# Optimization experiments

Measured on AMD Instinct MI355X. Metric: run time of the kernel, lower is better.

Reference implementation:

```python
import jax, jax.numpy as jnp
import numpy as np

NUM_HEADS = 12
SPARSITY = 0.5

def setup_inputs() -> dict:
    key = jax.random.key(0)
    ks = jax.random.split(key, 5)
    B, N, C = 16, 577, 768
    x = jax.random.normal(ks[0], (B, N, C), dtype=jnp.float32)
    x_original = jax.random.normal(ks[1], (B, N, C), dtype=jnp.float32)
    qkv_w = jax.random.normal(ks[2], (3 * C, C), dtype=jnp.float32) * (C ** -0.5)
    proj_w = jax.random.normal(ks[3], (C, C), dtype=jnp.float32) * (C ** -0.5)
    proj_b = jax.random.normal(ks[4], (C,), dtype=jnp.float32) * 0.01
    return {"x": x, "x_original": x_original, "qkv_w": qkv_w,
            "proj_w": proj_w, "proj_b": proj_b, "num_prop": 57}

def reference(x, x_original, qkv_w, proj_w, proj_b, num_prop):
    B, N, C = x.shape
    H = NUM_HEADS
    hd = C // H
    scale = hd ** -0.5
    # qkv projection (no bias): [B,N,3C] -> q,k,v each [B,H,N,hd]
    qkv = (x @ qkv_w.T).reshape(B, N, 3, H, hd).transpose(2, 0, 3, 1, 4)
    q, k, v = qkv[0], qkv[1], qkv[2]
    attn = jax.nn.softmax(jnp.einsum('bhnd,bhmd->bhnm', q * scale, k), axis=-1)
    # sparsity threshold: keep entries >= the int(N*N*sparsity)-th largest per (b,h)
    if SPARSITY < 1:
        flat = attn.reshape(B, H, N * N)
        desc = -jnp.sort(-flat, axis=-1)  # descending
        sigma = desc[:, :, int(N * N * SPARSITY)][:, :, None, None]
        attn = jnp.where(attn >= sigma, attn, jnp.zeros((), attn.dtype))
    if num_prop > 0:
        K = N - num_prop  # tokens kept (incl. CLS)
        # token importance: max over heads of attention diagonal (excluding CLS)
        diag = jnp.diagonal(attn, axis1=-2, axis2=-1)[:, :, 1:]  # [B,H,N-1]
        token_rank = jnp.argsort(-diag.max(axis=1), axis=1)      # [B,N-1] desc
        index_kept = token_rank[:, :N - 1 - num_prop] + 1        # [B,K-1]
        index_kept = jnp.concatenate(
            [jnp.zeros((B, 1), index_kept.dtype), index_kept], axis=1)  # [B,K]
        # gather kept query rows of attn: [B,H,K,N]
        idx = jnp.broadcast_to(index_kept[:, None, :, None], (B, H, K, N))
        attn_kept = jnp.take_along_axis(attn, idx, axis=2)
        x_original = jnp.take_along_axis(
            x_original, jnp.broadcast_to(index_kept[:, :, None], (B, K, C)), axis=1)
        out = jnp.einsum('bhkn,bhnd->bhkd', attn_kept, v)
        out = out.transpose(0, 2, 1, 3).reshape(B, K, C)
    else:
        out = jnp.einsum('bhnm,bhmd->bhnd', attn, v)
        out = out.transpose(0, 2, 1, 3).reshape(B, N, C)
    out = out @ proj_w.T + proj_b
    return (out, x_original)
```

## Files before the change

### kernel.cpp

```cpp
#include <hip/hip_runtime.h>
#include <cstdint>
#include <cstddef>


namespace {
constexpr int B_  = 16;
constexpr int N_  = 577;
constexpr int C_  = 768;
constexpr int H_  = 12;
constexpr int HD_ = 64;
constexpr int BH_ = B_ * H_;
constexpr int KK_ = N_ - 57;
constexpr unsigned KIDX_ = 166464u;
constexpr int M1_ = B_ * N_;
constexpr int M2_ = B_ * KK_;
}

__global__ __launch_bounds__(256) void qkv_gemm(
    const float* __restrict__ X, const float* __restrict__ W,
    float* __restrict__ qb, float* __restrict__ kb, float* __restrict__ vb) {
  __shared__ float Xs[64][37];
  __shared__ float Ws2[128][37];
  const int m0 = blockIdx.x * 64;
  const int n0 = blockIdx.y * 128;
  const int t = threadIdx.x;
  const int tx = t & 15, ty = t >> 4;
  const int sc = t & 7, sr = t >> 3;
  float acc[4][8] = {};
  for (int k0 = 0; k0 < 768; k0 += 32) {
    __syncthreads();
#pragma unroll
    for (int s = 0; s < 2; s++) {
      int r = sr + 32 * s;
      int gm = m0 + r;
      float4 v = make_float4(0.f, 0.f, 0.f, 0.f);
      if (gm < M1_) v = *(const float4*)&X[(size_t)gm * 768 + k0 + 4 * sc];
      Xs[r][4*sc+0] = v.x; Xs[r][4*sc+1] = v.y;
      Xs[r][4*sc+2] = v.z; Xs[r][4*sc+3] = v.w;
    }
#pragma unroll
    for (int s = 0; s < 4; s++) {
      int r = sr + 32 * s;
      float4 v = *(const float4*)&W[(size_t)(n0 + r) * 768 + k0 + 4 * sc];
      Ws2[r][4*sc+0] = v.x; Ws2[r][4*sc+1] = v.y;
      Ws2[r][4*sc+2] = v.z; Ws2[r][4*sc+3] = v.w;
    }
    __syncthreads();
#pragma unroll 8
    for (int kk = 0; kk < 32; kk++) {
      float a[4], bb[8];
#pragma unroll
      for (int i = 0; i < 4; i++) a[i] = Xs[tx + 16*i][kk];
#pragma unroll
      for (int j = 0; j < 8; j++) bb[j] = Ws2[8*ty + j][kk];
#pragma unroll
      for (int i = 0; i < 4; i++)
#pragma unroll
        for (int j = 0; j < 8; j++) acc[i][j] = __builtin_fmaf(a[i], bb[j], acc[i][j]);
    }
  }
  for (int i = 0; i < 4; i++) {
    int gm = m0 + tx + 16*i;
    if (gm >= M1_) continue;
    int b = gm / N_, n = gm % N_;
    for (int j = 0; j < 8; j++) {
      int gn = n0 + 8*ty + j;
      int which = gn / C_, rem = gn % C_;
      int h = rem >> 6, d = rem & 63;
      float* dst = (which == 0) ? qb : (which == 1) ? kb : vb;
      dst[(((size_t)(b * H_ + h)) * N_ + n) * HD_ + d] = acc[i][j];
    }
  }
}

__global__ __launch_bounds__(256) void attn_stats(
    const float* __restrict__ qb, const float* __restrict__ kb,
    float* __restrict__ rowmax_g, float* __restrict__ rowsum_g,
    float* __restrict__ ldiag) {
  __shared__ float Qs[64][69];
  __shared__ float Ksf[128 * 69];
  const int bh = blockIdx.x;
  const int q0 = blockIdx.y * 64;
  const int t = threadIdx.x;
  const int tx = t & 15, ty = t >> 4;
  {
    const int c = t & 15, r0 = t >> 4;
#pragma unroll
    for (int s = 0; s < 4; s++) {
      int r = r0 + 16 * s;
      int gq = q0 + r;
      float4 v = make_float4(0.f, 0.f, 0.f, 0.f);
      if (gq < N_) v = *(const float4*)&qb[((size_t)bh * N_ + gq) * HD_ + 4 * c];
      Qs[r][4*c+0] = v.x * 0.125f; Qs[r][4*c+1] = v.y * 0.125f;
      Qs[r][4*c+2] = v.z * 0.125f; Qs[r][4*c+3] = v.w * 0.125f;
    }
  }
  float m[4], ss[4];
#pragma unroll
  for (int i = 0; i < 4; i++) { m[i] = -INFINITY; ss[i] = 0.f; }
  for (int n0 = 0; n0 < N_; n0 += 128) {
    __syncthreads();
    {
      const int c = t & 15, r0 = t >> 4;
#pragma unroll
      for (int s = 0; s < 8; s++) {
        int r = r0 + 16 * s;
        int gn = n0 + r;
        float4 v = make_float4(0.f, 0.f, 0.f, 0.f);
        if (gn < N_) v = *(const float4*)&kb[((size_t)bh * N_ + gn) * HD_ + 4 * c];
        float* kr = &Ksf[r * 69];
        kr[4*c+0] = v.x; kr[4*c+1] = v.y; kr[4*c+2] = v.z; kr[4*c+3] = v.w;
      }
    }
    __syncthreads();
    float l[4][8];
#pragma unroll
    for (int i = 0; i < 4; i++)
#pragma unroll
      for (int j = 0; j < 8; j++) l[i][j] = 0.f;
#pragma unroll 8
    for (int d = 0; d < 64; d++) {
      float a[4], bb[8];
#pragma unroll
      for (int i = 0; i < 4; i++) a[i] = Qs[tx + 16*i][d];
#pragma unroll
      for (int j = 0; j < 8; j++) bb[j] = Ksf[(8*ty + j) * 69 + d];
#pragma unroll
      for (int i = 0; i < 4; i++)
#pragma unroll
        for (int j = 0; j < 8; j++) l[i][j] = __builtin_fmaf(a[i], bb[j], l[i][j]);
    }
    int cbase = n0 + 8 * ty;
    int cv = N_ - cbase; if (cv > 8) cv = 8;
    if (cv > 0) {
#pragma unroll
      for (int i = 0; i < 4; i++) {
        int gq = q0 + tx + 16*i;
        if (gq >= N_) continue;
        float tmax = -INFINITY;
        for (int j = 0; j < 8; j++) if (j < cv) tmax = fmaxf(tmax, l[i][j]);
        float mn = fmaxf(m[i], tmax);
        ss[i] *= expf(m[i] - mn);
        for (int j = 0; j < 8; j++) if (j < cv) ss[i] += expf(l[i][j] - mn);
        m[i] = mn;
        int dj = gq - cbase;
        if (dj >= 0 && dj < cv) ldiag[(size_t)bh * N_ + gq] = l[i][dj];
      }
    }
  }
  __syncthreads();
  float* Mred = Ksf;
  float* Sred = Ksf + 1024;
#pragma unroll
  for (int i = 0; i < 4; i++) {
    int row = tx + 16*i;
    Mred[row * 16 + ty] = m[i];
    Sred[row * 16 + ty] = ss[i];
  }
  __syncthreads();
  if (t < 64) {
    int gq = q0 + t;
    if (gq < N_) {
      float M = -INFINITY;
      for (int k = 0; k < 16; k++) M = fmaxf(M, Mred[t*16 + k]);
      float S = 0.f;
      for (int k = 0; k < 16; k++) S += expf(Mred[t*16+k] - M) * Sred[t*16+k];
      rowmax_g[(size_t)bh * N_ + gq] = M;
      rowsum_g[(size_t)bh * N_ + gq] = S;
    }
  }
}

template <int MODE>
__global__ __launch_bounds__(256) void hist_pass(
    const float* __restrict__ qb, const float* __restrict__ kb,
    const float* __restrict__ rowmax_g, const float* __restrict__ rowsum_g,
    const unsigned* __restrict__ pfx_in, unsigned* __restrict__ hist_out) {
  constexpr int HB = (MODE == 2) ? 256 : 4096;
  __shared__ float Qs[64][69];
  __shared__ float Ksf[128 * 69];
  __shared__ unsigned hloc[HB];
  const int bh = blockIdx.x;
  const int q0 = blockIdx.y * 64;
  const int t = threadIdx.x;
  const int tx = t & 15, ty = t >> 4;
  for (int i = t; i < HB; i += 256) hloc[i] = 0u;
  const unsigned pf = (MODE == 0) ? 0u : pfx_in[bh];
  {
    const int c = t & 15, r0 = t >> 4;
#pragma unroll
    for (int s = 0; s < 4; s++) {
      int r = r0 + 16 * s;
      int gq = q0 + r;
      float4 v = make_float4(0.f, 0.f, 0.f, 0.f);
      if (gq < N_) v = *(const float4*)&qb[((size_t)bh * N_ + gq) * HD_ + 4 * c];
      Qs[r][4*c+0] = v.x * 0.125f; Qs[r][4*c+1] = v.y * 0.125f;
      Qs[r][4*c+2] = v.z * 0.125f; Qs[r][4*c+3] = v.w * 0.125f;
    }
  }
  float M[4], inv[4];
#pragma unroll
  for (int i = 0; i < 4; i++) {
    int gq = q0 + tx + 16*i;
    if (gq < N_) {
      M[i] = rowmax_g[(size_t)bh * N_ + gq];
      inv[i] = 1.f / rowsum_g[(size_t)bh * N_ + gq];
    } else { M[i] = 0.f; inv[i] = 0.f; }
  }
  for (int n0 = 0; n0 < N_; n0 += 128) {
    __syncthreads();
    {
      const int c = t & 15, r0 = t >> 4;
#pragma unroll
      for (int s = 0; s < 8; s++) {
        int r = r0 + 16 * s;
        int gn = n0 + r;
        float4 v = make_float4(0.f, 0.f, 0.f, 0.f);
        if (gn < N_) v = *(const float4*)&kb[((size_t)bh * N_ + gn) * HD_ + 4 * c];
        float* kr = &Ksf[r * 69];
        kr[4*c+0] = v.x; kr[4*c+1] = v.y; kr[4*c+2] = v.z; kr[4*c+3] = v.w;
      }
    }
    __syncthreads();
    float l[4][8];
#pragma unroll
    for (int i = 0; i < 4; i++)
#pragma unroll
      for (int j = 0; j < 8; j++) l[i][j] = 0.f;
#pragma unroll 8
    for (int d = 0; d < 64; d++) {
      float a[4], bb[8];
#pragma unroll
      for (int i = 0; i < 4; i++) a[i] = Qs[tx + 16*i][d];
#pragma unroll
      for (int j = 0; j < 8; j++) bb[j] = Ksf[(8*ty + j) * 69 + d];
#pragma unroll
      for (int i = 0; i < 4; i++)
#pragma unroll
        for (int j = 0; j < 8; j++) l[i][j] = __builtin_fmaf(a[i], bb[j], l[i][j]);
    }
    int cbase = n0 + 8 * ty;
#pragma unroll
    for (int i = 0; i < 4; i++) {
      int gq = q0 + tx + 16 * i;
#pragma unroll
      for (int j = 0; j < 8; j++) {
        bool valid = (gq < N_) && (cbase + j < N_);
        if (MODE == 0) {
          unsigned bin = 0xFFFFu;
          if (valid) {
            float e = expf(l[i][j] - M[i]);
            float v = e * inv[i];
            bin = __float_as_uint(v) >> 20;
          }
          unsigned lead = (unsigned)__builtin_amdgcn_readfirstlane((int)bin);
          unsigned long long mm = __ballot(bin == lead);
          if (bin == lead) {
            if (lead != 0xFFFFu && (t & 63) == (__ffsll((unsigned long long)mm) - 1))
              atomicAdd(&hloc[lead], (unsigned)__popcll(mm));
          } else if (bin != 0xFFFFu) {
            atomicAdd(&hloc[bin], 1u);
          }
        } else if (valid) {
          float e = expf(l[i][j] - M[i]);
          float v = e * inv[i];
          unsigned bits = __float_as_uint(v);
          if (MODE == 1) {
            if ((bits >> 20) == pf) atomicAdd(&hloc[(bits >> 8) & 0xFFFu], 1u);
          } else {
            if ((bits >> 8) == pf) atomicAdd(&hloc[bits & 0xFFu], 1u);
          }
        }
      }
    }
  }
  __syncthreads();
  for (int i = t; i < HB; i += 256)
    if (hloc[i]) atomicAdd(&hist_out[(size_t)bh * HB + i], hloc[i]);
}

__global__ __launch_bounds__(64) void select_level(
    const unsigned* __restrict__ hist, int nbins,
    const unsigned* __restrict__ krem_in, const unsigned* __restrict__ pfx_in,
    unsigned* __restrict__ krem_out, unsigned* __restrict__ pfx_out, int shift) {
  const int bh = blockIdx.x;
  const int l = threadIdx.x;
  const int seg = nbins / 64;
  const unsigned krem = krem_in ? krem_in[bh] : KIDX_;
  const unsigned* hb = hist + (size_t)bh * nbins;
  __shared__ unsigned ps[64];
  unsigned psum = 0;
  int hi = nbins - 1 - l * seg;
  for (int i = 0; i < seg; i++) psum += hb[hi - i];
  ps[l] = psum;
  __syncthreads();
  if (l == 0) {
    unsigned cum = 0, before = 0;
    int bin = 0;
    for (int j = 0; j < 64; j++) {
      if (cum + ps[j] > krem) {
        unsigned c = cum;
        int hj = nbins - 1 - j * seg;
        for (int i = 0; i < seg; i++) {
          unsigned cnt = hb[hj - i];
          if (c + cnt > krem) { bin = hj - i; before = c; break; }
          c += cnt;
        }
        break;
      }
      cum += ps[j];
    }
    unsigned p = pfx_in ? pfx_in[bh] : 0u;
    pfx_out[bh] = (p << shift) | (unsigned)bin;
    krem_out[bh] = krem - before;
  }
}

__global__ __launch_bounds__(576) void rank_kernel(
    const float* __restrict__ ldiag, const float* __restrict__ rowmax_g,
    const float* __restrict__ rowsum_g, const unsigned* __restrict__ sigbits,
    int* __restrict__ kept) {
  const int b = blockIdx.x;
  const int i = threadIdx.x;
  __shared__ float sc[576];
  float s = 0.f;
  for (int h = 0; h < H_; h++) {
    int bh = b * H_ + h;
    float l = ldiag[(size_t)bh * N_ + (i + 1)];
    float M = rowmax_g[(size_t)bh * N_ + (i + 1)];
    float inv = 1.f / rowsum_g[(size_t)bh * N_ + (i + 1)];
    float e = expf(l - M);
    float v = e * inv;
    float sg = __uint_as_float(sigbits[bh]);
    if (v >= sg) s = fmaxf(s, v);
  }
  sc[i] = s;
  __syncthreads();
  int r = 0;
  for (int j = 0; j < 576; j++) {
    float sj = sc[j];
    if (sj > s || (sj == s && j < i)) r++;
  }
  if (r < KK_ - 1) kept[b * KK_ + r + 1] = i + 1;
  if (i == 0) kept[b * KK_] = 0;
}

__global__ __launch_bounds__(256) void gather_x(
    const float* __restrict__ xo, const int* __restrict__ kept,
    float* __restrict__ out2) {
  const int bp = blockIdx.x;
  const int b = bp / KK_, p = bp % KK_;
  const int src = kept[b * KK_ + p];
  const float* s = xo + ((size_t)b * N_ + src) * C_;
  float* d = out2 + (size_t)bp * C_;
  for (int c = threadIdx.x; c < C_; c += 256) d[c] = s[c];
}

__global__ __launch_bounds__(256) void av_kernel(
    const float* __restrict__ qb, const float* __restrict__ kb,
    const float* __restrict__ vb, const int* __restrict__ kept,
    const float* __restrict__ rowmax_g, const float* __restrict__ rowsum_g,
    const unsigned* __restrict__ sigbits, float* __restrict__ out1) {
  __shared__ float Qs[64][69];
  __shared__ float Ksf[64 * 69];
  __shared__ float Vs[64][69];
  __shared__ int ridx[64];
  __shared__ float Ml[64], Il[64];
  const int bh = blockIdx.x;
  const int p0 = blockIdx.y * 64;
  const int b = bh / H_, h = bh % H_;
  const float sigma = __uint_as_float(sigbits[bh]);
  const int t = threadIdx.x;
  const int tx = t & 15, ty = t >> 4;
  if (t < 64) {
    int pp = p0 + t;
    int r = (pp < KK_) ? kept[b * KK_ + pp] : 0;
    ridx[t] = r;
    Ml[t] = rowmax_g[(size_t)bh * N_ + r];
    Il[t] = 1.f / rowsum_g[(size_t)bh * N_ + r];
  }
  __syncthreads();
  {
    const int c = t & 15, r0 = t >> 4;
#pragma unroll
    for (int s = 0; s < 4; s++) {
      int r = r0 + 16 * s;
      int gq = ridx[r];
      float4 v = *(const float4*)&qb[((size_t)bh * N_ + gq) * HD_ + 4 * c];
      Qs[r][4*c+0] = v.x * 0.125f; Qs[r][4*c+1] = v.y * 0.125f;
      Qs[r][4*c+2] = v.z * 0.125f; Qs[r][4*c+3] = v.w * 0.125f;
    }
  }
  float M[4], inv[4];
#pragma unroll
  for (int i = 0; i < 4; i++) { int row = tx + 16*i; M[i] = Ml[row]; inv[i] = Il[row]; }
  float acc[4][4] = {};
  for (int n0 = 0; n0 < N_; n0 += 64) {
    __syncthreads();
    {
      const int c = t & 15, r0 = t >> 4;
#pragma unroll
      for (int s = 0; s < 4; s++) {
        int r = r0 + 16 * s;
        int gn = n0 + r;
        float4 kv = make_float4(0.f, 0.f, 0.f, 0.f);
        float4 vv = make_float4(0.f, 0.f, 0.f, 0.f);
        if (gn < N_) {
          kv = *(const float4*)&kb[((size_t)bh * N_ + gn) * HD_ + 4 * c];
          vv = *(const float4*)&vb[((size_t)bh * N_ + gn) * HD_ + 4 * c];
        }
        float* kr = &Ksf[r * 69];
        kr[4*c+0] = kv.x; kr[4*c+1] = kv.y; kr[4*c+2] = kv.z; kr[4*c+3] = kv.w;
        Vs[r][4*c+0] = vv.x; Vs[r][4*c+1] = vv.y;
        Vs[r][4*c+2] = vv.z; Vs[r][4*c+3] = vv.w;
      }
    }
    __syncthreads();
    float l[4][4];
#pragma unroll
    for (int i = 0; i < 4; i++)
#pragma unroll
      for (int j = 0; j < 4; j++) l[i][j] = 0.f;
#pragma unroll 8
    for (int d = 0; d < 64; d++) {
      float a[4], bb[4];
#pragma unroll
      for (int i = 0; i < 4; i++) a[i] = Qs[tx + 16*i][d];
#pragma unroll
      for (int j = 0; j < 4; j++) bb[j] = Ksf[(4*ty + j) * 69 + d];
#pragma unroll
      for (int i = 0; i < 4; i++)
#pragma unroll
        for (int j = 0; j < 4; j++) l[i][j] = __builtin_fmaf(a[i], bb[j], l[i][j]);
    }
    __syncthreads();
#pragma unroll
    for (int i = 0; i < 4; i++) {
#pragma unroll
      for (int j = 0; j < 4; j++) {
        float e = expf(l[i][j] - M[i]);
        float v = e * inv[i];
        float pm = (v >= sigma) ? v : 0.f;
        Ksf[(tx + 16*i) * 69 + 4*ty + j] = pm;
      }
    }
    __syncthreads();
#pragma unroll 8
    for (int n = 0; n < 64; n++) {
      float pa[4], vv[4];
#pragma unroll
      for (int i = 0; i < 4; i++) pa[i] = Ksf[(tx + 16*i) * 69 + n];
#pragma unroll
      for (int j = 0; j < 4; j++) vv[j] = Vs[n][4*ty + j];
#pragma unroll
      for (int i = 0; i < 4; i++)
#pragma unroll
        for (int j = 0; j < 4; j++) acc[i][j] = __builtin_fmaf(pa[i], vv[j], acc[i][j]);
    }
  }
#pragma unroll
  for (int i = 0; i < 4; i++) {
    int pp = p0 + tx + 16*i;
    if (pp >= KK_) continue;
#pragma unroll
    for (int j = 0; j < 4; j++) {
      out1[((size_t)(b * KK_ + pp)) * C_ + h * HD_ + 4*ty + j] = acc[i][j];
    }
  }
}

__global__ __launch_bounds__(256) void proj_gemm(
    const float* __restrict__ Xi, const float* __restrict__ W,
    const float* __restrict__ bias, float* __restrict__ out) {
  __shared__ float Xs[64][37];
  __shared__ float Ws2[128][37];
  const int m0 = blockIdx.x * 64;
  const int n0 = blockIdx.y * 128;
  const int t = threadIdx.x;
  const int tx = t & 15, ty = t >> 4;
  const int sc = t & 7, sr = t >> 3;
  float acc[4][8] = {};
  for (int k0 = 0; k0 < 768; k0 += 32) {
    __syncthreads();
#pragma unroll
    for (int s = 0; s < 2; s++) {
      int r = sr + 32 * s;
      float4 v = *(const float4*)&Xi[(size_t)(m0 + r) * 768 + k0 + 4 * sc];
      Xs[r][4*sc+0] = v.x; Xs[r][4*sc+1] = v.y;
      Xs[r][4*sc+2] = v.z; Xs[r][4*sc+3] = v.w;
    }
#pragma unroll
    for (int s = 0; s < 4; s++) {
      int r = sr + 32 * s;
      float4 v = *(const float4*)&W[(size_t)(n0 + r) * 768 + k0 + 4 * sc];
      Ws2[r][4*sc+0] = v.x; Ws2[r][4*sc+1] = v.y;
      Ws2[r][4*sc+2] = v.z; Ws2[r][4*sc+3] = v.w;
    }
    __syncthreads();
#pragma unroll 8
    for (int kk = 0; kk < 32; kk++) {
      float a[4], bb[8];
#pragma unroll
      for (int i = 0; i < 4; i++) a[i] = Xs[tx + 16*i][kk];
#pragma unroll
      for (int j = 0; j < 8; j++) bb[j] = Ws2[8*ty + j][kk];
#pragma unroll
      for (int i = 0; i < 4; i++)
#pragma unroll
        for (int j = 0; j < 8; j++) acc[i][j] = __builtin_fmaf(a[i], bb[j], acc[i][j]);
    }
  }
  for (int i = 0; i < 4; i++) {
    int gm = m0 + tx + 16*i;
    for (int j = 0; j < 8; j++) {
      int gn = n0 + 8*ty + j;
      out[(size_t)gm * C_ + gn] = acc[i][j] + bias[gn];
    }
  }
}

extern "C" void kernel_launch(void* const* d_in, const int* in_sizes, int n_in,
                              void* d_out, int out_size, void* d_ws, size_t ws_size,
                              hipStream_t stream) {
  (void)in_sizes; (void)n_in; (void)out_size; (void)ws_size;
  const float* x    = (const float*)d_in[0];
  const float* xo   = (const float*)d_in[1];
  const float* qkvw = (const float*)d_in[2];
  const float* pw   = (const float*)d_in[3];
  const float* pb   = (const float*)d_in[4];

  char* ws = (char*)d_ws;
  size_t off = 0;
  auto alloc = [&](size_t bytes) -> char* {
    char* p = ws + off;
    off += (bytes + 255) & ~(size_t)255;
    return p;
  };
  const size_t szQ    = (size_t)BH_ * N_ * HD_ * 4;
  const size_t szOut1 = (size_t)M2_ * C_ * 4;
  const size_t szRow  = (size_t)BH_ * N_ * 4;
  const size_t szH12  = (size_t)BH_ * 4096 * 4;
  const size_t szH3   = (size_t)BH_ * 256 * 4;

  float* qb     = (float*)alloc(szQ);
  float* kb     = (float*)alloc(szQ);
  float* vb     = (float*)alloc(szQ);
  float* out1   = (float*)alloc(szOut1);
  float* ldiag  = (float*)alloc(szRow);
  float* rowmax = (float*)alloc(szRow);
  float* rowsum = (float*)alloc(szRow);
  unsigned* hist1 = (unsigned*)alloc(szH12);
  unsigned* hist2 = (unsigned*)alloc(szH12);
  unsigned* hist3 = (unsigned*)alloc(szH3);
  unsigned* pfx1  = (unsigned*)alloc(BH_ * 4);
  unsigned* krem1 = (unsigned*)alloc(BH_ * 4);
  unsigned* pfx2  = (unsigned*)alloc(BH_ * 4);
  unsigned* krem2 = (unsigned*)alloc(BH_ * 4);
  unsigned* pfx3  = (unsigned*)alloc(BH_ * 4);
  unsigned* krem3 = (unsigned*)alloc(BH_ * 4);
  int* kept       = (int*)alloc((size_t)B_ * KK_ * 4);

  hipMemsetAsync(hist1, 0, szH12, stream);
  hipMemsetAsync(hist2, 0, szH12, stream);
  hipMemsetAsync(hist3, 0, szH3, stream);

  qkv_gemm<<<dim3(145, 18), 256, 0, stream>>>(x, qkvw, qb, kb, vb);
  attn_stats<<<dim3(BH_, 10), 256, 0, stream>>>(qb, kb, rowmax, rowsum, ldiag);
  hist_pass<0><<<dim3(BH_, 10), 256, 0, stream>>>(qb, kb, rowmax, rowsum, nullptr, hist1);
  select_level<<<BH_, 64, 0, stream>>>(hist1, 4096, nullptr, nullptr, krem1, pfx1, 12);
  hist_pass<1><<<dim3(BH_, 10), 256, 0, stream>>>(qb, kb, rowmax, rowsum, pfx1, hist2);
  select_level<<<BH_, 64, 0, stream>>>(hist2, 4096, krem1, pfx1, krem2, pfx2, 12);
  hist_pass<2><<<dim3(BH_, 10), 256, 0, stream>>>(qb, kb, rowmax, rowsum, pfx2, hist3);
  select_level<<<BH_, 64, 0, stream>>>(hist3, 256, krem2, pfx2, krem3, pfx3, 8);
  rank_kernel<<<B_, 576, 0, stream>>>(ldiag, rowmax, rowsum, pfx3, kept);

  float* outp = (float*)d_out;
  gather_x<<<M2_, 256, 0, stream>>>(xo, kept, outp + (size_t)M2_ * C_);
  av_kernel<<<dim3(BH_, 9), 256, 0, stream>>>(qb, kb, vb, kept, rowmax, rowsum, pfx3, out1);
  proj_gemm<<<dim3(130, 6), 256, 0, stream>>>(out1, pw, pb, outp);
}
```

Before: 1.983 ms.

## Vectorize shared-memory tiles with float4 loads across all GEMM-like kernels

Changes shared-memory tiles from odd-padded (37/69) rows to 16-byte aligned rows of 68 floats, so global-to-shared stores and inner-loop reads use float4. The thread-to-column mapping becomes strided (ty + 16*j) instead of contiguous, and the QKV/proj GEMMs now step K by 64 instead of 32. The aim is fewer LDS instructions per FMA in the QK^T, PV and projection loops. Float4 reads with a 68-float stride can cause LDS bank conflicts, and the changed reduction order may shift numerics slightly.

```diff
diff --git a/kernel.cpp b/kernel.cpp
--- a/kernel.cpp
+++ b/kernel.cpp
@@ -16,55 +16,62 @@
 constexpr int M2_ = B_ * KK_;
 }
 
+__device__ __forceinline__ void fma4(const float4& a, const float4& b, float& acc) {
+  acc = __builtin_fmaf(a.x, b.x, acc);
+  acc = __builtin_fmaf(a.y, b.y, acc);
+  acc = __builtin_fmaf(a.z, b.z, acc);
+  acc = __builtin_fmaf(a.w, b.w, acc);
+}
+
 __global__ __launch_bounds__(256) void qkv_gemm(
     const float* __restrict__ X, const float* __restrict__ W,
     float* __restrict__ qb, float* __restrict__ kb, float* __restrict__ vb) {
-  __shared__ float Xs[64][37];
-  __shared__ float Ws2[128][37];
+  __shared__ __align__(16) float Xs[64][68];
+  __shared__ __align__(16) float Ws2[128][68];
   const int m0 = blockIdx.x * 64;
   const int n0 = blockIdx.y * 128;
   const int t = threadIdx.x;
   const int tx = t & 15, ty = t >> 4;
-  const int sc = t & 7, sr = t >> 3;
   float acc[4][8] = {};
-  for (int k0 = 0; k0 < 768; k0 += 32) {
-    __syncthreads();
-#pragma unroll
-    for (int s = 0; s < 2; s++) {
-      int r = sr + 32 * s;
-      int gm = m0 + r;
-      float4 v = make_float4(0.f, 0.f, 0.f, 0.f);
-      if (gm < M1_) v = *(const float4*)&X[(size_t)gm * 768 + k0 + 4 * sc];
-      Xs[r][4*sc+0] = v.x; Xs[r][4*sc+1] = v.y;
-      Xs[r][4*sc+2] = v.z; Xs[r][4*sc+3] = v.w;
-    }
-#pragma unroll
-    for (int s = 0; s < 4; s++) {
-      int r = sr + 32 * s;
-      float4 v = *(const float4*)&W[(size_t)(n0 + r) * 768 + k0 + 4 * sc];
-      Ws2[r][4*sc+0] = v.x; Ws2[r][4*sc+1] = v.y;
-      Ws2[r][4*sc+2] = v.z; Ws2[r][4*sc+3] = v.w;
-    }
-    __syncthreads();
-#pragma unroll 8
-    for (int kk = 0; kk < 32; kk++) {
-      float a[4], bb[8];
-#pragma unroll
-      for (int i = 0; i < 4; i++) a[i] = Xs[tx + 16*i][kk];
-#pragma unroll
-      for (int j = 0; j < 8; j++) bb[j] = Ws2[8*ty + j][kk];
+  for (int k0 = 0; k0 < 768; k0 += 64) {
+    __syncthreads();
+    {
+      const int c = t & 15, r0 = t >> 4;
+#pragma unroll
+      for (int s = 0; s < 4; s++) {
+        int r = r0 + 16 * s;
+        int gm = m0 + r;
+        float4 v = make_float4(0.f, 0.f, 0.f, 0.f);
+        if (gm < M1_) v = *(const float4*)&X[(size_t)gm * 768 + k0 + 4 * c];
+        *(float4*)&Xs[r][4 * c] = v;
+      }
+#pragma unroll
+      for (int s = 0; s < 8; s++) {
+        int r = r0 + 16 * s;
+        float4 v = *(const float4*)&W[(size_t)(n0 + r) * 768 + k0 + 4 * c];
+        *(float4*)&Ws2[r][4 * c] = v;
+      }
+    }
+    __syncthreads();
+#pragma unroll 2
+    for (int d4 = 0; d4 < 16; d4++) {
+      float4 a4[4], b4[8];
+#pragma unroll
+      for (int i = 0; i < 4; i++) a4[i] = *(const float4*)&Xs[tx + 16 * i][4 * d4];
+#pragma unroll
+      for (int j = 0; j < 8; j++) b4[j] = *(const float4*)&Ws2[ty + 16 * j][4 * d4];
 #pragma unroll
       for (int i = 0; i < 4; i++)
 #pragma unroll
-        for (int j = 0; j < 8; j++) acc[i][j] = __builtin_fmaf(a[i], bb[j], acc[i][j]);
+        for (int j = 0; j < 8; j++) fma4(a4[i], b4[j], acc[i][j]);
     }
   }
   for (int i = 0; i < 4; i++) {
-    int gm = m0 + tx + 16*i;
+    int gm = m0 + tx + 16 * i;
     if (gm >= M1_) continue;
     int b = gm / N_, n = gm % N_;
     for (int j = 0; j < 8; j++) {
-      int gn = n0 + 8*ty + j;
+      int gn = n0 + ty + 16 * j;
       int which = gn / C_, rem = gn % C_;
       int h = rem >> 6, d = rem & 63;
       float* dst = (which == 0) ? qb : (which == 1) ? kb : vb;
@@ -77,8 +84,8 @@
     const float* __restrict__ qb, const float* __restrict__ kb,
     float* __restrict__ rowmax_g, float* __restrict__ rowsum_g,
     float* __restrict__ ldiag) {
-  __shared__ float Qs[64][69];
-  __shared__ float Ksf[128 * 69];
+  __shared__ __align__(16) float Qs[64][68];
+  __shared__ __align__(16) float Ksf[128][68];
   const int bh = blockIdx.x;
   const int q0 = blockIdx.y * 64;
   const int t = threadIdx.x;
@@ -91,8 +98,8 @@
       int gq = q0 + r;
       float4 v = make_float4(0.f, 0.f, 0.f, 0.f);
       if (gq < N_) v = *(const float4*)&qb[((size_t)bh * N_ + gq) * HD_ + 4 * c];
-      Qs[r][4*c+0] = v.x * 0.125f; Qs[r][4*c+1] = v.y * 0.125f;
-      Qs[r][4*c+2] = v.z * 0.125f; Qs[r][4*c+3] = v.w * 0.125f;
+      v.x *= 0.125f; v.y *= 0.125f; v.z *= 0.125f; v.w *= 0.125f;
+      *(float4*)&Qs[r][4 * c] = v;
     }
   }
   float m[4], ss[4];
@@ -108,8 +115,7 @@
         int gn = n0 + r;
         float4 v = make_float4(0.f, 0.f, 0.f, 0.f);
         if (gn < N_) v = *(const float4*)&kb[((size_t)bh * N_ + gn) * HD_ + 4 * c];
-        float* kr = &Ksf[r * 69];
-        kr[4*c+0] = v.x; kr[4*c+1] = v.y; kr[4*c+2] = v.z; kr[4*c+3] = v.w;
+        *(float4*)&Ksf[r][4 * c] = v;
       }
     }
     __syncthreads();
@@ -118,42 +124,44 @@
     for (int i = 0; i < 4; i++)
 #pragma unroll
       for (int j = 0; j < 8; j++) l[i][j] = 0.f;
-#pragma unroll 8
-    for (int d = 0; d < 64; d++) {
-      float a[4], bb[8];
-#pragma unroll
-      for (int i = 0; i < 4; i++) a[i] = Qs[tx + 16*i][d];
-#pragma unroll
-      for (int j = 0; j < 8; j++) bb[j] = Ksf[(8*ty + j) * 69 + d];
+#pragma unroll 2
+    for (int d4 = 0; d4 < 16; d4++) {
+      float4 a4[4], b4[8];
+#pragma unroll
+      for (int i = 0; i < 4; i++) a4[i] = *(const float4*)&Qs[tx + 16 * i][4 * d4];
+#pragma unroll
+      for (int j = 0; j < 8; j++) b4[j] = *(const float4*)&Ksf[ty + 16 * j][4 * d4];
 #pragma unroll
       for (int i = 0; i < 4; i++)
 #pragma unroll
-        for (int j = 0; j < 8; j++) l[i][j] = __builtin_fmaf(a[i], bb[j], l[i][j]);
-    }
-    int cbase = n0 + 8 * ty;
-    int cv = N_ - cbase; if (cv > 8) cv = 8;
-    if (cv > 0) {
-#pragma unroll
-      for (int i = 0; i < 4; i++) {
-        int gq = q0 + tx + 16*i;
-        if (gq >= N_) continue;
-        float tmax = -INFINITY;
-        for (int j = 0; j < 8; j++) if (j < cv) tmax = fmaxf(tmax, l[i][j]);
-        float mn = fmaxf(m[i], tmax);
-        ss[i] *= expf(m[i] - mn);
-        for (int j = 0; j < 8; j++) if (j < cv) ss[i] += expf(l[i][j] - mn);
-        m[i] = mn;
-        int dj = gq - cbase;
-        if (dj >= 0 && dj < cv) ldiag[(size_t)bh * N_ + gq] = l[i][dj];
-      }
+        for (int j = 0; j < 8; j++) fma4(a4[i], b4[j], l[i][j]);
+    }
+#pragma unroll
+    for (int i = 0; i < 4; i++) {
+      int gq = q0 + tx + 16 * i;
+      float tmax = -INFINITY;
+#pragma unroll
+      for (int j = 0; j < 8; j++)
+        if (n0 + ty + 16 * j < N_) tmax = fmaxf(tmax, l[i][j]);
+      float mn = fmaxf(m[i], tmax);
+      ss[i] *= expf(m[i] - mn);
+#pragma unroll
+      for (int j = 0; j < 8; j++) {
+        int col = n0 + ty + 16 * j;
+        if (col < N_) {
+          ss[i] += expf(l[i][j] - mn);
+          if (col == gq) ldiag[(size_t)bh * N_ + gq] = l[i][j];
+        }
+      }
+      m[i] = mn;
     }
   }
   __syncthreads();
-  float* Mred = Ksf;
-  float* Sred = Ksf + 1024;
+  float* Mred = &Ksf[0][0];
+  float* Sred = &Ksf[0][0] + 1024;
 #pragma unroll
   for (int i = 0; i < 4; i++) {
-    int row = tx + 16*i;
+    int row = tx + 16 * i;
     Mred[row * 16 + ty] = m[i];
     Sred[row * 16 + ty] = ss[i];
   }
@@ -162,9 +170,9 @@
     int gq = q0 + t;
     if (gq < N_) {
       float M = -INFINITY;
-      for (int k = 0; k < 16; k++) M = fmaxf(M, Mred[t*16 + k]);
+      for (int k = 0; k < 16; k++) M = fmaxf(M, Mred[t * 16 + k]);
       float S = 0.f;
-      for (int k = 0; k < 16; k++) S += expf(Mred[t*16+k] - M) * Sred[t*16+k];
+      for (int k = 0; k < 16; k++) S += expf(Mred[t * 16 + k] - M) * Sred[t * 16 + k];
       rowmax_g[(size_t)bh * N_ + gq] = M;
       rowsum_g[(size_t)bh * N_ + gq] = S;
     }
@@ -177,8 +185,8 @@
     const float* __restrict__ rowmax_g, const float* __restrict__ rowsum_g,
     const unsigned* __restrict__ pfx_in, unsigned* __restrict__ hist_out) {
   constexpr int HB = (MODE == 2) ? 256 : 4096;
-  __shared__ float Qs[64][69];
-  __shared__ float Ksf[128 * 69];
+  __shared__ __align__(16) float Qs[64][68];
+  __shared__ __align__(16) float Ksf[128][68];
   __shared__ unsigned hloc[HB];
   const int bh = blockIdx.x;
   const int q0 = blockIdx.y * 64;
@@ -194,14 +202,14 @@
       int gq = q0 + r;
       float4 v = make_float4(0.f, 0.f, 0.f, 0.f);
       if (gq < N_) v = *(const float4*)&qb[((size_t)bh * N_ + gq) * HD_ + 4 * c];
-      Qs[r][4*c+0] = v.x * 0.125f; Qs[r][4*c+1] = v.y * 0.125f;
-      Qs[r][4*c+2] = v.z * 0.125f; Qs[r][4*c+3] = v.w * 0.125f;
+      v.x *= 0.125f; v.y *= 0.125f; v.z *= 0.125f; v.w *= 0.125f;
+      *(float4*)&Qs[r][4 * c] = v;
     }
   }
   float M[4], inv[4];
 #pragma unroll
   for (int i = 0; i < 4; i++) {
-    int gq = q0 + tx + 16*i;
+    int gq = q0 + tx + 16 * i;
     if (gq < N_) {
       M[i] = rowmax_g[(size_t)bh * N_ + gq];
       inv[i] = 1.f / rowsum_g[(size_t)bh * N_ + gq];
@@ -217,8 +225,7 @@
         int gn = n0 + r;
         float4 v = make_float4(0.f, 0.f, 0.f, 0.f);
         if (gn < N_) v = *(const float4*)&kb[((size_t)bh * N_ + gn) * HD_ + 4 * c];
-        float* kr = &Ksf[r * 69];
-        kr[4*c+0] = v.x; kr[4*c+1] = v.y; kr[4*c+2] = v.z; kr[4*c+3] = v.w;
+        *(float4*)&Ksf[r][4 * c] = v;
       }
     }
     __syncthreads();
@@ -227,25 +234,24 @@
     for (int i = 0; i < 4; i++)
 #pragma unroll
       for (int j = 0; j < 8; j++) l[i][j] = 0.f;
-#pragma unroll 8
-    for (int d = 0; d < 64; d++) {
-      float a[4], bb[8];
-#pragma unroll
-      for (int i = 0; i < 4; i++) a[i] = Qs[tx + 16*i][d];
-#pragma unroll
-      for (int j = 0; j < 8; j++) bb[j] = Ksf[(8*ty + j) * 69 + d];
+#pragma unroll 2
+    for (int d4 = 0; d4 < 16; d4++) {
+      float4 a4[4], b4[8];
+#pragma unroll
+      for (int i = 0; i < 4; i++) a4[i] = *(const float4*)&Qs[tx + 16 * i][4 * d4];
+#pragma unroll
+      for (int j = 0; j < 8; j++) b4[j] = *(const float4*)&Ksf[ty + 16 * j][4 * d4];
 #pragma unroll
       for (int i = 0; i < 4; i++)
 #pragma unroll
-        for (int j = 0; j < 8; j++) l[i][j] = __builtin_fmaf(a[i], bb[j], l[i][j]);
-    }
-    int cbase = n0 + 8 * ty;
+        for (int j = 0; j < 8; j++) fma4(a4[i], b4[j], l[i][j]);
+    }
 #pragma unroll
     for (int i = 0; i < 4; i++) {
       int gq = q0 + tx + 16 * i;
 #pragma unroll
       for (int j = 0; j < 8; j++) {
-        bool valid = (gq < N_) && (cbase + j < N_);
+        bool valid = (gq < N_) && (n0 + ty + 16 * j < N_);
         if (MODE == 0) {
           unsigned bin = 0xFFFFu;
           if (valid) {
@@ -361,9 +367,9 @@
     const float* __restrict__ vb, const int* __restrict__ kept,
     const float* __restrict__ rowmax_g, const float* __restrict__ rowsum_g,
     const unsigned* __restrict__ sigbits, float* __restrict__ out1) {
-  __shared__ float Qs[64][69];
-  __shared__ float Ksf[64 * 69];
-  __shared__ float Vs[64][69];
+  __shared__ __align__(16) float Qs[64][68];
+  __shared__ __align__(16) float Ksf[64][68];
+  __shared__ __align__(16) float Vs[64][68];
   __shared__ int ridx[64];
   __shared__ float Ml[64], Il[64];
   const int bh = blockIdx.x;
@@ -387,13 +393,13 @@
       int r = r0 + 16 * s;
       int gq = ridx[r];
       float4 v = *(const float4*)&qb[((size_t)bh * N_ + gq) * HD_ + 4 * c];
-      Qs[r][4*c+0] = v.x * 0.125f; Qs[r][4*c+1] = v.y * 0.125f;
-      Qs[r][4*c+2] = v.z * 0.125f; Qs[r][4*c+3] = v.w * 0.125f;
+      v.x *= 0.125f; v.y *= 0.125f; v.z *= 0.125f; v.w *= 0.125f;
+      *(float4*)&Qs[r][4 * c] = v;
     }
   }
   float M[4], inv[4];
 #pragma unroll
-  for (int i = 0; i < 4; i++) { int row = tx + 16*i; M[i] = Ml[row]; inv[i] = Il[row]; }
+  for (int i = 0; i < 4; i++) { int row = tx + 16 * i; M[i] = Ml[row]; inv[i] = Il[row]; }
   float acc[4][4] = {};
   for (int n0 = 0; n0 < N_; n0 += 64) {
     __syncthreads();
@@ -409,10 +415,8 @@
           kv = *(const float4*)&kb[((size_t)bh * N_ + gn) * HD_ + 4 * c];
           vv = *(const float4*)&vb[((size_t)bh * N_ + gn) * HD_ + 4 * c];
         }
-        float* kr = &Ksf[r * 69];
-        kr[4*c+0] = kv.x; kr[4*c+1] = kv.y; kr[4*c+2] = kv.z; kr[4*c+3] = kv.w;
-        Vs[r][4*c+0] = vv.x; Vs[r][4*c+1] = vv.y;
-        Vs[r][4*c+2] = vv.z; Vs[r][4*c+3] = vv.w;
+        *(float4*)&Ksf[r][4 * c] = kv;
+        *(float4*)&Vs[r][4 * c] = vv;
       }
     }
     __syncthreads();
@@ -421,99 +425,107 @@
     for (int i = 0; i < 4; i++)
 #pragma unroll
       for (int j = 0; j < 4; j++) l[i][j] = 0.f;
-#pragma unroll 8
-    for (int d = 0; d < 64; d++) {
-      float a[4], bb[4];
-#pragma unroll
-      for (int i = 0; i < 4; i++) a[i] = Qs[tx + 16*i][d];
-#pragma unroll
-      for (int j = 0; j < 4; j++) bb[j] = Ksf[(4*ty + j) * 69 + d];
+#pragma unroll 4
+    for (int d4 = 0; d4 < 16; d4++) {
+      float4 a4[4], b4[4];
+#pragma unroll
+      for (int i = 0; i < 4; i++) a4[i] = *(const float4*)&Qs[tx + 16 * i][4 * d4];
+#pragma unroll
+      for (int j = 0; j < 4; j++) b4[j] = *(const float4*)&Ksf[4 * ty + j][4 * d4];
 #pragma unroll
       for (int i = 0; i < 4; i++)
 #pragma unroll
-        for (int j = 0; j < 4; j++) l[i][j] = __builtin_fmaf(a[i], bb[j], l[i][j]);
+        for (int j = 0; j < 4; j++) fma4(a4[i], b4[j], l[i][j]);
     }
     __syncthreads();
 #pragma unroll
     for (int i = 0; i < 4; i++) {
+      float4 pv4;
+      float* pp = (float*)&pv4;
 #pragma unroll
       for (int j = 0; j < 4; j++) {
         float e = expf(l[i][j] - M[i]);
         float v = e * inv[i];
-        float pm = (v >= sigma) ? v : 0.f;
-        Ksf[(tx + 16*i) * 69 + 4*ty + j] = pm;
-      }
-    }
-    __syncthreads();
-#pragma unroll 8
-    for (int n = 0; n < 64; n++) {
-      float pa[4], vv[4];
-#pragma unroll
-      for (int i = 0; i < 4; i++) pa[i] = Ksf[(tx + 16*i) * 69 + n];
-#pragma unroll
-      for (int j = 0; j < 4; j++) vv[j] = Vs[n][4*ty + j];
-#pragma unroll
-      for (int i = 0; i < 4; i++)
-#pragma unroll
-        for (int j = 0; j < 4; j++) acc[i][j] = __builtin_fmaf(pa[i], vv[j], acc[i][j]);
+        pp[j] = (v >= sigma) ? v : 0.f;
+      }
+      *(float4*)&Ksf[tx + 16 * i][4 * ty] = pv4;
+    }
+    __syncthreads();
+#pragma unroll 4
+    for (int nb = 0; nb < 16; nb++) {
+      float4 pa4[4];
+#pragma unroll
+      for (int i = 0; i < 4; i++) pa4[i] = *(const float4*)&Ksf[tx + 16 * i][4 * nb];
+#pragma unroll
+      for (int e = 0; e < 4; e++) {
+        float4 vv4 = *(const float4*)&Vs[4 * nb + e][4 * ty];
+        const float* pa = (const float*)&pa4[0];
+#pragma unroll
+        for (int i = 0; i < 4; i++) {
+          float pvv = ((const float*)&pa4[i])[e];
+          acc[i][0] = __builtin_fmaf(pvv, vv4.x, acc[i][0]);
+          acc[i][1] = __builtin_fmaf(pvv, vv4.y, acc[i][1]);
+          acc[i][2] = __builtin_fmaf(pvv, vv4.z, acc[i][2]);
+          acc[i][3] = __builtin_fmaf(pvv, vv4.w, acc[i][3]);
+        }
+        (void)pa;
+      }
     }
   }
 #pragma unroll
   for (int i = 0; i < 4; i++) {
-    int pp = p0 + tx + 16*i;
+    int pp = p0 + tx + 16 * i;
     if (pp >= KK_) continue;
-#pragma unroll
-    for (int j = 0; j < 4; j++) {
-      out1[((size_t)(b * KK_ + pp)) * C_ + h * HD_ + 4*ty + j] = acc[i][j];
-    }
+    float4 o = make_float4(acc[i][0], acc[i][1], acc[i][2], acc[i][3]);
+    *(float4*)&out1[((size_t)(b * KK_ + pp)) * C_ + h * HD_ + 4 * ty] = o;
   }
 }
 
 __global__ __launch_bounds__(256) void proj_gemm(
     const float* __restrict__ Xi, const float* __restrict__ W,
     const float* __restrict__ bias, float* __restrict__ out) {
-  __shared__ float Xs[64][37];
-  __shared__ float Ws2[128][37];
+  __shared__ __align__(16) float Xs[64][68];
+  __shared__ __align__(16) float Ws2[128][68];
   const int m0 = blockIdx.x * 64;
   const int n0 = blockIdx.y * 128;
   const int t = threadIdx.x;
   const int tx = t & 15, ty = t >> 4;
-  const int sc = t & 7, sr = t >> 3;
   float acc[4][8] = {};
-  for (int k0 = 0; k0 < 768; k0 += 32) {
-    __syncthreads();
-#pragma unroll
-    for (int s = 0; s < 2; s++) {
-      int r = sr + 32 * s;
-      float4 v = *(const float4*)&Xi[(size_t)(m0 + r) * 768 + k0 + 4 * sc];
-      Xs[r][4*sc+0] = v.x; Xs[r][4*sc+1] = v.y;
-      Xs[r][4*sc+2] = v.z; Xs[r][4*sc+3] = v.w;
-    }
-#pragma unroll
-    for (int s = 0; s < 4; s++) {
-      int r = sr + 32 * s;
-      float4 v = *(const float4*)&W[(size_t)(n0 + r) * 768 + k0 + 4 * sc];
-      Ws2[r][4*sc+0] = v.x; Ws2[r][4*sc+1] = v.y;
-      Ws2[r][4*sc+2] = v.z; Ws2[r][4*sc+3] = v.w;
-    }
-    __syncthreads();
-#pragma unroll 8
-    for (int kk = 0; kk < 32; kk++) {
-      float a[4], bb[8];
-#pragma unroll
-      for (int i = 0; i < 4; i++) a[i] = Xs[tx + 16*i][kk];
-#pragma unroll
-      for (int j = 0; j < 8; j++) bb[j] = Ws2[8*ty + j][kk];
+  for (int k0 = 0; k0 < 768; k0 += 64) {
+    __syncthreads();
+    {
+      const int c = t & 15, r0 = t >> 4;
+#pragma unroll
+      for (int s = 0; s < 4; s++) {
+        int r = r0 + 16 * s;
+        float4 v = *(const float4*)&Xi[(size_t)(m0 + r) * 768 + k0 + 4 * c];
+        *(float4*)&Xs[r][4 * c] = v;
+      }
+#pragma unroll
+      for (int s = 0; s < 8; s++) {
+        int r = r0 + 16 * s;
+        float4 v = *(const float4*)&W[(size_t)(n0 + r) * 768 + k0 + 4 * c];
+        *(float4*)&Ws2[r][4 * c] = v;
+      }
+    }
+    __syncthreads();
+#pragma unroll 2
+    for (int d4 = 0; d4 < 16; d4++) {
+      float4 a4[4], b4[8];
+#pragma unroll
+      for (int i = 0; i < 4; i++) a4[i] = *(const float4*)&Xs[tx + 16 * i][4 * d4];
+#pragma unroll
+      for (int j = 0; j < 8; j++) b4[j] = *(const float4*)&Ws2[ty + 16 * j][4 * d4];
 #pragma unroll
       for (int i = 0; i < 4; i++)
 #pragma unroll
-        for (int j = 0; j < 8; j++) acc[i][j] = __builtin_fmaf(a[i], bb[j], acc[i][j]);
+        for (int j = 0; j < 8; j++) fma4(a4[i], b4[j], acc[i][j]);
     }
   }
   for (int i = 0; i < 4; i++) {
-    int gm = m0 + tx + 16*i;
+    int gm = m0 + tx + 16 * i;
     for (int j = 0; j < 8; j++) {
-      int gn = n0 + 8*ty + j;
+      int gn = n0 + ty + 16 * j;
       out[(size_t)gm * C_ + gn] = acc[i][j] + bias[gn];
     }
   }
```

New measurement: 1.801 ms. 9.2% less time.
